# Performance work log

Hardware: AMD Instinct MI355X
Metric: run time of the kernel (lower is better)

Reference implementation:

```python
import jax, jax.numpy as jnp
import numpy as np

# ---- static config (mirrors Net.__init__) ----
N_NODES, N_EDGES = 4000, 20000
N_PROTS, D = 919, 512            # node_emb: Embedding(919, 512); F_in = D (divide_input=False)
TOWERS, F_OUT = 4, D // 4        # F_out = out_channels // towers = 128
EDGE_D = 50
N_GRAPHS, N_CLASSES = 32, 10
N_LAYERS = 2
EPS_BN, EPS_STD = 1e-5, 1e-5

# deg histogram passed to PNAConv; only avg_deg['log'] matters for the scalers used
DEG_HIST = np.array([0., 800., 1200., 900., 600., 300., 150., 50.])
AVG_DEG_LOG = float((np.log(np.arange(DEG_HIST.size) + 1.0) * DEG_HIST).sum() / DEG_HIST.sum())


def setup_inputs() -> dict:
    key = jax.random.key(0)
    ks = jax.random.split(key, 16)
    g = lambda i, shape, s=0.05: (jax.random.normal(ks[i], shape, jnp.float32) * s)
    return dict(
        node_emb_w=g(0, (N_PROTS, D), 0.1),
        edge_emb_w=g(1, (2, EDGE_D), 0.1),
        pe_w=g(2, (2, D)), pe_b=jnp.zeros((D,), jnp.float32),
        edge_enc_w=g(3, (N_LAYERS, EDGE_D, D)), edge_enc_b=jnp.zeros((N_LAYERS, D), jnp.float32),
        pre_w=g(4, (N_LAYERS, TOWERS, 3 * D, D)), pre_b=jnp.zeros((N_LAYERS, TOWERS, D), jnp.float32),
        post_w=g(5, (N_LAYERS, TOWERS, 13 * D, F_OUT)), post_b=jnp.zeros((N_LAYERS, TOWERS, F_OUT), jnp.float32),
        lin_w=g(6, (N_LAYERS, D, D)), lin_b=jnp.zeros((N_LAYERS, D), jnp.float32),
        bn_gamma=jnp.ones((N_LAYERS, D), jnp.float32), bn_beta=jnp.zeros((N_LAYERS, D), jnp.float32),
        acts=jax.random.normal(ks[7], (N_NODES, 2), jnp.float32),
        fc1_w=g(8, (D, 2 * D)), fc1_b=jnp.zeros((2 * D,), jnp.float32),
        fc_out_w=g(9, (2 * D, N_CLASSES)), fc_out_b=jnp.zeros((N_CLASSES,), jnp.float32),
        prelu_a=jnp.float32(0.25),
        global_idx=jax.random.randint(ks[10], (N_NODES,), 0, N_PROTS),
        sign=jax.random.randint(ks[11], (N_EDGES,), 0, 2),
        edge_index=jax.random.randint(ks[12], (2, N_EDGES), 0, N_NODES),
        batch=jnp.sort(jax.random.randint(ks[13], (N_NODES,), 0, N_GRAPHS)),
    )


def _pna_layer(x, src, dst, e, pre_w, pre_b, post_w, post_b, lin_w, lin_b):
    # x: [N, D], e: [E, D] (edge_encoder output), pre_w: [T, 3D, D], post_w: [T, 13D, F_OUT]
    N, E = x.shape[0], src.shape[0]
    # pre-NN on cat([x_i, x_j, edge_attr]) expressed as split matmuls (pre_layers=1 -> single Linear)
    Wi, Wj, We = pre_w[:, :D], pre_w[:, D:2 * D], pre_w[:, 2 * D:]
    m = (jnp.einsum('ef,tfd->etd', x[dst], Wi)
         + jnp.einsum('ef,tfd->etd', x[src], Wj)
         + jnp.einsum('ef,tfd->etd', e, We) + pre_b)          # [E, T, D]
    # multi-aggregation at destination nodes: mean / min / max / std
    cnt = jax.ops.segment_sum(jnp.ones((E,), m.dtype), dst, N)  # in-degree
    has = (cnt > 0)[:, None, None]
    deg = jnp.maximum(cnt, 1.0)[:, None, None]                  # clamp(1) as in PyG
    s1 = jax.ops.segment_sum(m, dst, N)
    s2 = jax.ops.segment_sum(m * m, dst, N)
    mean = s1 / deg
    std = jnp.sqrt(jax.nn.relu(s2 / deg - mean * mean) + EPS_STD)
    mn = jnp.where(has, jax.ops.segment_min(m, dst, N), 0.0)
    mx = jnp.where(has, jax.ops.segment_max(m, dst, N), 0.0)
    agg = jnp.concatenate([mean, mn, mx, std], axis=-1)         # [N, T, 4D]
    # degree scalers: identity, amplification, attenuation
    amp = jnp.log(deg + 1.0) / AVG_DEG_LOG
    out = jnp.concatenate([agg, agg * amp, agg / amp], axis=-1)  # [N, T, 12D]
    # post-NN on cat([x, out]) as split matmuls (post_layers=1)
    Wx, Wo = post_w[:, :D], post_w[:, D:]
    o = (jnp.einsum('nf,tfd->ntd', x, Wx)
         + jnp.einsum('ntf,tfd->ntd', out, Wo) + post_b)        # [N, T, F_OUT]
    return o.reshape(N, TOWERS * F_OUT) @ lin_w + lin_b         # [N, D]


def reference(node_emb_w, edge_emb_w, pe_w, pe_b, edge_enc_w, edge_enc_b,
              pre_w, pre_b, post_w, post_b, lin_w, lin_b, bn_gamma, bn_beta,
              acts, fc1_w, fc1_b, fc_out_w, fc_out_b, prelu_a,
              global_idx, sign, edge_index, batch):
    src, dst = edge_index[0], edge_index[1]
    x = node_emb_w[global_idx] + (acts @ pe_w + pe_b)           # node_emb + PostEncoding
    ea = edge_emb_w[sign]                                       # [E, 50]
    for l in range(N_LAYERS):
        e = ea @ edge_enc_w[l] + edge_enc_b[l]                  # shared edge encoder
        h = _pna_layer(x, src, dst, e, pre_w[l], pre_b[l], post_w[l], post_b[l], lin_w[l], lin_b[l])
        mu = h.mean(axis=0)
        var = ((h - mu) ** 2).mean(axis=0)                      # training-mode BatchNorm (biased var)
        x = jax.nn.relu(bn_gamma[l] * (h - mu) * jax.lax.rsqrt(var + EPS_BN) + bn_beta[l])
    pooled = jax.ops.segment_sum(x, batch, N_GRAPHS)            # global_add_pool
    z = pooled @ fc1_w + fc1_b
    z = jnp.where(z > 0, z, prelu_a * z)                        # PReLU
    logits = z @ fc_out_w + fc_out_b
    return jax.nn.log_softmax(logits, axis=-1)
```

## Files before the change

kernel.cpp:

```cpp
#include <hip/hip_runtime.h>
#include <hip/hip_bf16.h>
#include <float.h>

#define NN 4000
#define NE 20000
#define DD 512
#define NT 4
#define FO 128
#define NG 32
#define NC 10
#define XGW 4096
#define AVGLOG 1.2548916493836102f
#define EPS_STD_ 1e-5f
#define EPS_BN_ 1e-5f

typedef __bf16 bf16x8 __attribute__((ext_vector_type(8)));
typedef float  f32x4  __attribute__((ext_vector_type(4)));

__device__ __forceinline__ void async_copy16(const void* g, void* l) {
    __builtin_amdgcn_global_load_lds((const __attribute__((address_space(1))) void*)g,
                                     (__attribute__((address_space(3))) void*)l, 16, 0, 0);
}

__global__ __launch_bounds__(256) void k_xg(const __bf16* __restrict__ XB, const __bf16* __restrict__ WCAT,
                                            const float* __restrict__ pb,
                                            __bf16* __restrict__ XG, float* __restrict__ OF,
                                            float* __restrict__ BN, float* __restrict__ PL, int zero_pl) {
    const int m0 = blockIdx.y * 128, n0 = blockIdx.x * 128;
    __shared__ __bf16 As[128 * 32];
    __shared__ __bf16 Bs[128 * 32];
    const int tid = threadIdx.x;
    const int wave = tid >> 6, lane = tid & 63;
    const int wm = (wave >> 1) * 64, wn = (wave & 1) * 64;
    const int fr = lane & 15, fq = lane >> 4;
    const int fk = fq * 8;
    const int srow = lane >> 2, skc = (lane & 3) * 8;

    f32x4 acc[4][4];
    const f32x4 zero = {0.f, 0.f, 0.f, 0.f};
#pragma unroll
    for (int i = 0; i < 4; ++i)
#pragma unroll
        for (int j = 0; j < 4; ++j) acc[i][j] = zero;

    for (int k0 = 0; k0 < 512; k0 += 32) {
#pragma unroll
        for (int q = 0; q < 2; ++q) {
            const int row = wave * 32 + q * 16 + srow;
            int ar = m0 + row; if (ar > NN - 1) ar = NN - 1;
            async_copy16(XB + (size_t)ar * 512 + k0 + skc, As + wave * 1024 + q * 512);
            async_copy16(WCAT + (size_t)(n0 + row) * 512 + k0 + skc, Bs + wave * 1024 + q * 512);
        }
        __syncthreads();
        bf16x8 af[4], bfr[4];
#pragma unroll
        for (int mi = 0; mi < 4; ++mi) af[mi]  = *(const bf16x8*)(As + (wm + mi * 16 + fr) * 32 + fk);
#pragma unroll
        for (int ni = 0; ni < 4; ++ni) bfr[ni] = *(const bf16x8*)(Bs + (wn + ni * 16 + fr) * 32 + fk);
#pragma unroll
        for (int mi = 0; mi < 4; ++mi)
#pragma unroll
            for (int ni = 0; ni < 4; ++ni)
                acc[mi][ni] = __builtin_amdgcn_mfma_f32_16x16x32_bf16(af[mi], bfr[ni], acc[mi][ni], 0, 0, 0);
        __syncthreads();
    }
    if (n0 < 4096) {
#pragma unroll
        for (int mi = 0; mi < 4; ++mi) {
#pragma unroll
            for (int ni = 0; ni < 4; ++ni) {
                const int col = n0 + wn + ni * 16 + fr;
                const int rb = m0 + wm + mi * 16 + fq * 4;
#pragma unroll
                for (int r = 0; r < 4; ++r) {
                    const int rowc = rb + r;
                    if (rowc < NN) XG[(size_t)rowc * XGW + col] = (__bf16)acc[mi][ni][r];
                }
            }
        }
    } else {
        const int ocb = n0 - 4096;
#pragma unroll
        for (int mi = 0; mi < 4; ++mi) {
#pragma unroll
            for (int ni = 0; ni < 4; ++ni) {
                const int oc = ocb + wn + ni * 16 + fr;
                const float bv = pb[oc];
                const int rb = m0 + wm + mi * 16 + fq * 4;
#pragma unroll
                for (int r = 0; r < 4; ++r) {
                    const int rowc = rb + r;
                    if (rowc < NN) OF[(size_t)rowc * 512 + oc] = acc[mi][ni][r] + bv;
                }
            }
        }
    }
    if (blockIdx.x == 32 && blockIdx.y == 0) {
        BN[tid] = 0.f; BN[256 + tid] = 0.f; BN[512 + tid] = 0.f; BN[768 + tid] = 0.f;
        if (zero_pl)
            for (int i = tid; i < NG * DD; i += 256) PL[i] = 0.f;
    }
}

__global__ __launch_bounds__(256) void k_gw(const __bf16* __restrict__ AB, const __bf16* __restrict__ WTT,
                                            const float* __restrict__ amp, const float* __restrict__ ramp,
                                            float* __restrict__ OF) {
    const int t = blockIdx.z & 3, kh = blockIdx.z >> 2;
    const int xg = blockIdx.x;
    const int m0 = blockIdx.y * 128;
    const __bf16* A  = AB  + (size_t)t * 2048 + (size_t)kh * 1024;
    const __bf16* BT = WTT + (size_t)t * 384 * 2048 + (size_t)xg * 128 * 2048 + (size_t)kh * 1024;
    __shared__ __bf16 As[128 * 32];
    __shared__ __bf16 Bs[128 * 32];
    const int tid = threadIdx.x;
    const int wave = tid >> 6, lane = tid & 63;
    const int wm = (wave >> 1) * 64, wn = (wave & 1) * 64;
    const int fr = lane & 15, fq = lane >> 4;
    const int fk = fq * 8;
    const int srow = lane >> 2, skc = (lane & 3) * 8;

    f32x4 acc[4][4];
    const f32x4 zero = {0.f, 0.f, 0.f, 0.f};
#pragma unroll
    for (int i = 0; i < 4; ++i)
#pragma unroll
        for (int j = 0; j < 4; ++j) acc[i][j] = zero;

    for (int k0 = 0; k0 < 1024; k0 += 32) {
#pragma unroll
        for (int q = 0; q < 2; ++q) {
            const int row = wave * 32 + q * 16 + srow;
            int ar = m0 + row; if (ar > NN - 1) ar = NN - 1;
            async_copy16(A + (size_t)ar * 8192 + k0 + skc, As + wave * 1024 + q * 512);
            async_copy16(BT + (size_t)row * 2048 + k0 + skc, Bs + wave * 1024 + q * 512);
        }
        __syncthreads();
        bf16x8 af[4], bfr[4];
#pragma unroll
        for (int mi = 0; mi < 4; ++mi) af[mi]  = *(const bf16x8*)(As + (wm + mi * 16 + fr) * 32 + fk);
#pragma unroll
        for (int ni = 0; ni < 4; ++ni) bfr[ni] = *(const bf16x8*)(Bs + (wn + ni * 16 + fr) * 32 + fk);
#pragma unroll
        for (int mi = 0; mi < 4; ++mi)
#pragma unroll
            for (int ni = 0; ni < 4; ++ni)
                acc[mi][ni] = __builtin_amdgcn_mfma_f32_16x16x32_bf16(af[mi], bfr[ni], acc[mi][ni], 0, 0, 0);
        __syncthreads();
    }
#pragma unroll
    for (int mi = 0; mi < 4; ++mi) {
        const int rb = m0 + wm + mi * 16 + fq * 4;
#pragma unroll
        for (int r = 0; r < 4; ++r) {
            const int row = rb + r;
            if (row < NN) {
                const float w = (xg == 0) ? 1.0f : (xg == 1 ? amp[row] : ramp[row]);
                float* orow = OF + (size_t)row * 512 + t * 128;
#pragma unroll
                for (int ni = 0; ni < 4; ++ni)
                    atomicAdd(orow + wn + ni * 16 + fr, acc[mi][ni][r] * w);
            }
        }
    }
}

__global__ __launch_bounds__(256) void k_lin(const float* __restrict__ OF, const __bf16* __restrict__ WLINT,
                                             const float* __restrict__ bl, float* __restrict__ H,
                                             float* __restrict__ BN) {
    const int n0c = blockIdx.x * 128, m0 = blockIdx.y * 64;
    __shared__ __bf16 As[64 * 32];
    __shared__ __bf16 Bs[128 * 32];
    __shared__ float bnS[128], bnQ[128];
    const int tid = threadIdx.x;
    if (tid < 128) { bnS[tid] = 0.f; bnQ[tid] = 0.f; }
    const int wave = tid >> 6, lane = tid & 63;
    const int wr = wave >> 1, wc = wave & 1;
    const int fr = lane & 15, fq = lane >> 4;
    f32x4 acc[2][4];
    const f32x4 zero = {0.f, 0.f, 0.f, 0.f};
#pragma unroll
    for (int i = 0; i < 2; ++i)
#pragma unroll
        for (int j = 0; j < 4; ++j) acc[i][j] = zero;

    const int ar = tid >> 2, akc = (tid & 3) * 8;
    int arow = m0 + ar; if (arow > NN - 1) arow = NN - 1;
    const float* asrc = OF + (size_t)arow * 512;
    for (int k0 = 0; k0 < 512; k0 += 32) {
        float4 f0 = *(const float4*)(asrc + k0 + akc);
        float4 f1 = *(const float4*)(asrc + k0 + akc + 4);
        bf16x8 av;
        av[0] = (__bf16)f0.x; av[1] = (__bf16)f0.y; av[2] = (__bf16)f0.z; av[3] = (__bf16)f0.w;
        av[4] = (__bf16)f1.x; av[5] = (__bf16)f1.y; av[6] = (__bf16)f1.z; av[7] = (__bf16)f1.w;
        *(bf16x8*)(As + ar * 32 + akc) = av;
#pragma unroll
        for (int i = 0; i < 2; ++i) {
            const int cb = tid + 256 * i;
            const int br = cb >> 2, bkc = (cb & 3) * 8;
            async_copy16(WLINT + (size_t)(n0c + br) * 512 + k0 + bkc, Bs + cb * 8);
        }
        __syncthreads();
        bf16x8 a[2], b[4];
#pragma unroll
        for (int mi = 0; mi < 2; ++mi) a[mi] = *(const bf16x8*)(As + (wr * 32 + mi * 16 + fr) * 32 + fq * 8);
#pragma unroll
        for (int ni = 0; ni < 4; ++ni) b[ni] = *(const bf16x8*)(Bs + (wc * 64 + ni * 16 + fr) * 32 + fq * 8);
#pragma unroll
        for (int mi = 0; mi < 2; ++mi)
#pragma unroll
            for (int ni = 0; ni < 4; ++ni)
                acc[mi][ni] = __builtin_amdgcn_mfma_f32_16x16x32_bf16(a[mi], b[ni], acc[mi][ni], 0, 0, 0);
        __syncthreads();
    }
#pragma unroll
    for (int ni = 0; ni < 4; ++ni) {
        const int lc = wc * 64 + ni * 16 + fr;
        const int col = n0c + lc;
        const float bv = bl[col];
        float s = 0.f, q = 0.f;
#pragma unroll
        for (int mi = 0; mi < 2; ++mi) {
#pragma unroll
            for (int r = 0; r < 4; ++r) {
                const int rowc = m0 + wr * 32 + mi * 16 + fq * 4 + r;
                if (rowc < NN) {
                    const float v = acc[mi][ni][r] + bv;
                    H[(size_t)rowc * 512 + col] = v;
                    s += v; q += v * v;
                }
            }
        }
        atomicAdd(&bnS[lc], s); atomicAdd(&bnQ[lc], q);
    }
    __syncthreads();
    if (tid < 128) {
        atomicAdd(&BN[n0c + tid], bnS[tid]);
        atomicAdd(&BN[512 + n0c + tid], bnQ[tid]);
    }
}

__device__ __forceinline__ void tr32(const float* __restrict__ S, int sld,
                                     __bf16* __restrict__ D, int dld, int tx, int ty) {
    __shared__ float t[32][33];
    const int y0 = ty * 4;
#pragma unroll
    for (int i = 0; i < 4; ++i) t[y0 + i][tx] = S[(size_t)(y0 + i) * sld + tx];
    __syncthreads();
#pragma unroll
    for (int i = 0; i < 4; ++i) D[(size_t)(y0 + i) * dld + tx] = (__bf16)t[tx][y0 + i];
}

__global__ __launch_bounds__(256) void k_tr(const float* __restrict__ pw, const float* __restrict__ pow_,
                                            const float* __restrict__ lw,
                                            const float* __restrict__ eemb, const float* __restrict__ eew,
                                            const float* __restrict__ eeb, const float* __restrict__ pb,
                                            __bf16* __restrict__ WCAT, __bf16* __restrict__ WTT,
                                            __bf16* __restrict__ WLINT, float* __restrict__ EM) {
    const int id = blockIdx.x;
    const int tx = threadIdx.x & 31, ty = threadIdx.x >> 5;
    if (id < 2048) {
        const int z = id >> 8, r = id & 255;
        const int t = z & 3, half = z >> 2;
        const int x = r & 15, y = r >> 4;
        const float* S = pw + ((size_t)(t * 1536 + half * 512 + y * 32)) * 512 + x * 32;
        __bf16* D = WCAT + ((size_t)(half * 2048 + t * 512 + x * 32)) * 512 + y * 32;
        tr32(S, 512, D, 512, tx, ty);
    } else if (id < 2304) {
        const int id3 = id - 2048;
        const int t = id3 >> 6, r = id3 & 63;
        const int x = r & 3, y = r >> 2;
        const float* S = pow_ + ((size_t)(t * 6656 + y * 32)) * 128 + x * 32;
        __bf16* D = WCAT + ((size_t)(4096 + t * 128 + x * 32)) * 512 + y * 32;
        tr32(S, 128, D, 512, tx, ty);
    } else if (id < 5376) {
        const int id4 = id - 2304;
        const int z = id4 >> 8, r = id4 & 255;
        const int t = z / 3, w = z % 3;
        const int x = r & 3, y = r >> 2;
        const float* S = pow_ + ((size_t)(t * 6656 + 512 + w * 2048 + y * 32)) * 128 + x * 32;
        __bf16* D = WTT + (size_t)t * 384 * 2048 + ((size_t)(w * 128 + x * 32)) * 2048 + y * 32;
        tr32(S, 128, D, 2048, tx, ty);
    } else if (id < 5632) {
        const int r = id - 5376;
        const int x = r & 15, y = r >> 4;
        const float* S = lw + (size_t)y * 32 * 512 + x * 32;
        __bf16* D = WLINT + (size_t)x * 32 * 512 + y * 32;
        tr32(S, 512, D, 512, tx, ty);
    } else {
        __shared__ float eks[512];
        __shared__ float part[4][64];
        const int tid = threadIdx.x;
        const int id5 = id - 5632;
        const int k = id5 >> 5;
        const int g0 = (id5 & 31) * 64;
#pragma unroll
        for (int h = 0; h < 2; ++h) {
            const int f = tid + h * 256;
            float s = eeb[f];
            for (int c = 0; c < 50; ++c) s += eemb[k * 50 + c] * eew[(size_t)c * 512 + f];
            eks[f] = s;
        }
        __syncthreads();
        const int wave = tid >> 6, lane = tid & 63;
        const int g = g0 + lane;
        const int t = g >> 9, d = g & 511;
        const float* Wp = pw + ((size_t)(t * 1536 + 1024)) * 512 + d;
        float s = 0.f;
        const int f0 = wave * 128;
#pragma unroll 4
        for (int f = f0; f < f0 + 128; ++f) s += eks[f] * Wp[(size_t)f * 512];
        part[wave][lane] = s;
        __syncthreads();
        if (tid < 64) {
            const int gg = g0 + tid;
            EM[k * 2048 + gg] = pb[gg] + part[0][tid] + part[1][tid] + part[2][tid] + part[3][tid];
        }
    }
}

__global__ void k_count(const int* __restrict__ dst, int* __restrict__ cnt) {
    int e = blockIdx.x * 256 + threadIdx.x;
    if (e < NE) atomicAdd(&cnt[dst[e]], 1);
}

__global__ __launch_bounds__(1024) void k_scan_bx(const int* __restrict__ cnt, int* __restrict__ offs,
                                                  float* __restrict__ amp, float* __restrict__ ramp,
                                                  const float* __restrict__ nemb, const float* __restrict__ acts,
                                                  const float* __restrict__ pew, const float* __restrict__ peb,
                                                  const int* __restrict__ gidx, __bf16* __restrict__ XB) {
    const int t = threadIdx.x;
    if (blockIdx.x == 0) {
        __shared__ int part[1024];
        const int base = t * 4;
        int loc[4]; int s = 0;
#pragma unroll
        for (int i = 0; i < 4; ++i) { int v = (base + i < NN) ? cnt[base + i] : 0; loc[i] = s; s += v; }
        part[t] = s;
        __syncthreads();
        for (int o = 1; o < 1024; o <<= 1) {
            int v = (t >= o) ? part[t - o] : 0;
            __syncthreads();
            part[t] += v;
            __syncthreads();
        }
        const int pre = (t > 0) ? part[t - 1] : 0;
#pragma unroll
        for (int i = 0; i < 4; ++i) if (base + i < NN) offs[base + i] = pre + loc[i];
        if (t == 1023) offs[NN] = part[1023];
        for (int n = t; n < NN; n += 1024) {
            float deg = fmaxf((float)cnt[n], 1.0f);
            float a = logf(deg + 1.0f) / AVGLOG;
            amp[n] = a; ramp[n] = 1.0f / a;
        }
    } else {
        const int idx = (blockIdx.x - 1) * 1024 + t;
        const int n = idx >> 9, d = idx & 511;
        float v = nemb[(size_t)gidx[n] * DD + d] + acts[n * 2] * pew[d] + acts[n * 2 + 1] * pew[DD + d] + peb[d];
        XB[idx] = (__bf16)v;
    }
}

__global__ void k_fill(const int* __restrict__ src, const int* __restrict__ dst,
                       const int* __restrict__ sgn, const int* __restrict__ offs,
                       int* __restrict__ fill, int* __restrict__ esrc, int* __restrict__ esgn) {
    int e = blockIdx.x * 256 + threadIdx.x;
    if (e < NE) {
        int d = dst[e];
        int pos = offs[d] + atomicAdd(&fill[d], 1);
        esrc[pos] = src[e];
        esgn[pos] = sgn[e];
    }
}

__global__ __launch_bounds__(256) void k_agg(const __bf16* __restrict__ XG, const float* __restrict__ EM,
                                             const int* __restrict__ offs, const int* __restrict__ cnt,
                                             const int* __restrict__ esrc, const int* __restrict__ esgn,
                                             __bf16* __restrict__ AB) {
    const int n = blockIdx.x;
    const int g = threadIdx.x * 8;
    float xid[8], em0[8], em1[8];
    {
        bf16x8 xb = *(const bf16x8*)(XG + (size_t)n * XGW + g);
#pragma unroll
        for (int i = 0; i < 8; ++i) xid[i] = (float)xb[i];
    }
    *(float4*)&em0[0] = *(const float4*)&EM[g];
    *(float4*)&em0[4] = *(const float4*)&EM[g + 4];
    *(float4*)&em1[0] = *(const float4*)&EM[2048 + g];
    *(float4*)&em1[4] = *(const float4*)&EM[2048 + g + 4];
    float s1[8], s2[8], mn[8], mx[8];
#pragma unroll
    for (int i = 0; i < 8; ++i) { s1[i] = 0.f; s2[i] = 0.f; mn[i] = FLT_MAX; mx[i] = -FLT_MAX; }
    const int j0 = offs[n], j1 = offs[n + 1];
    for (int j = j0; j < j1; ++j) {
        const int s = esrc[j];
        const int sg = esgn[j];
        bf16x8 xv = *(const bf16x8*)(XG + (size_t)s * XGW + 2048 + g);
#pragma unroll
        for (int i = 0; i < 8; ++i) {
            float m = xid[i] + (float)xv[i] + (sg ? em1[i] : em0[i]);
            s1[i] += m; s2[i] += m * m;
            mn[i] = fminf(mn[i], m); mx[i] = fmaxf(mx[i], m);
        }
    }
    const int c = cnt[n];
    const float deg = fmaxf((float)c, 1.0f);
    const float rdeg = 1.0f / deg;
    bf16x8 vmean, vmn, vmx, vsd;
#pragma unroll
    for (int i = 0; i < 8; ++i) {
        float mean = s1[i] * rdeg;
        float var = s2[i] * rdeg - mean * mean;
        float sd = sqrtf(fmaxf(var, 0.f) + EPS_STD_);
        float mnv = (c == 0) ? 0.f : mn[i];
        float mxv = (c == 0) ? 0.f : mx[i];
        vmean[i] = (__bf16)mean; vmn[i] = (__bf16)mnv; vmx[i] = (__bf16)mxv; vsd[i] = (__bf16)sd;
    }
    const int t = g >> 9, d = g & 511;
    __bf16* base = AB + (size_t)n * 8192 + (size_t)t * 2048 + d;
    *(bf16x8*)(base + 0 * DD) = vmean;
    *(bf16x8*)(base + 1 * DD) = vmn;
    *(bf16x8*)(base + 2 * DD) = vmx;
    *(bf16x8*)(base + 3 * DD) = vsd;
}

__global__ void k_bnapply(const float* __restrict__ H, const float* __restrict__ BN,
                          const float* __restrict__ gamma, const float* __restrict__ beta,
                          __bf16* __restrict__ XB, float* __restrict__ PL,
                          const int* __restrict__ batch, int last) {
    int idx = blockIdx.x * 256 + threadIdx.x;
    int n = idx >> 9, d = idx & 511;
    float mu = BN[d] * (1.0f / NN);
    float var = BN[512 + d] * (1.0f / NN) - mu * mu;
    float v = gamma[d] * (H[idx] - mu) * rsqrtf(var + EPS_BN_) + beta[d];
    v = fmaxf(v, 0.f);
    if (last) atomicAdd(&PL[(size_t)batch[n] * DD + d], v);
    else XB[idx] = (__bf16)v;
}

__global__ __launch_bounds__(128) void k_fc1(const float* __restrict__ PL, const float* __restrict__ W1,
                                             const float* __restrict__ b1, const float* __restrict__ pa,
                                             float* __restrict__ Z) {
    const int g = blockIdx.x >> 3;
    const int j = (blockIdx.x & 7) * 128 + threadIdx.x;
    __shared__ float pl[512];
    for (int i = threadIdx.x; i < 512; i += 128) pl[i] = PL[(size_t)g * 512 + i];
    __syncthreads();
    const float* w = W1 + j;
    float s0 = 0.f, s1 = 0.f, s2 = 0.f, s3 = 0.f;
#pragma unroll 2
    for (int f = 0; f < 512; f += 4) {
        s0 += pl[f + 0] * w[(size_t)(f + 0) * 1024];
        s1 += pl[f + 1] * w[(size_t)(f + 1) * 1024];
        s2 += pl[f + 2] * w[(size_t)(f + 2) * 1024];
        s3 += pl[f + 3] * w[(size_t)(f + 3) * 1024];
    }
    float s = b1[j] + ((s0 + s1) + (s2 + s3));
    const float a = *pa;
    Z[(size_t)g * 1024 + j] = s > 0.f ? s : a * s;
}

__global__ __launch_bounds__(64) void k_out(const float* __restrict__ Z, const float* __restrict__ Wo,
                                            const float* __restrict__ bo, float* __restrict__ out) {
    const int g = blockIdx.x, t = threadIdx.x;
    float part[NC];
#pragma unroll
    for (int c = 0; c < NC; ++c) part[c] = 0.f;
    for (int f = t; f < 1024; f += 64) {
        const float zv = Z[(size_t)g * 1024 + f];
#pragma unroll
        for (int c = 0; c < NC; ++c) part[c] += zv * Wo[(size_t)f * NC + c];
    }
#pragma unroll
    for (int off = 32; off > 0; off >>= 1)
#pragma unroll
        for (int c = 0; c < NC; ++c) part[c] += __shfl_down(part[c], off);
    if (t == 0) {
        float lg[NC], mxv = -FLT_MAX;
#pragma unroll
        for (int c = 0; c < NC; ++c) { lg[c] = part[c] + bo[c]; mxv = fmaxf(mxv, lg[c]); }
        float se = 0.f;
#pragma unroll
        for (int c = 0; c < NC; ++c) se += expf(lg[c] - mxv);
        const float lse = mxv + logf(se);
#pragma unroll
        for (int c = 0; c < NC; ++c) out[g * NC + c] = lg[c] - lse;
    }
}

extern "C" void kernel_launch(void* const* d_in, const int* in_sizes, int n_in,
                              void* d_out, int out_size, void* d_ws, size_t ws_size,
                              hipStream_t stream) {
    const float* node_emb_w = (const float*)d_in[0];
    const float* edge_emb_w = (const float*)d_in[1];
    const float* pe_w   = (const float*)d_in[2];
    const float* pe_b   = (const float*)d_in[3];
    const float* edge_enc_w = (const float*)d_in[4];
    const float* edge_enc_b = (const float*)d_in[5];
    const float* pre_w  = (const float*)d_in[6];
    const float* pre_b  = (const float*)d_in[7];
    const float* post_w = (const float*)d_in[8];
    const float* post_b = (const float*)d_in[9];
    const float* lin_w  = (const float*)d_in[10];
    const float* lin_b  = (const float*)d_in[11];
    const float* bn_gamma = (const float*)d_in[12];
    const float* bn_beta  = (const float*)d_in[13];
    const float* acts   = (const float*)d_in[14];
    const float* fc1_w  = (const float*)d_in[15];
    const float* fc1_b  = (const float*)d_in[16];
    const float* fc_out_w = (const float*)d_in[17];
    const float* fc_out_b = (const float*)d_in[18];
    const float* prelu_a  = (const float*)d_in[19];
    const int* global_idx = (const int*)d_in[20];
    const int* sgn        = (const int*)d_in[21];
    const int* edge_index = (const int*)d_in[22];
    const int* batch      = (const int*)d_in[23];
    float* out = (float*)d_out;

    char* W = (char*)d_ws;
    size_t off = 0;
    auto alloc = [&](size_t bytes) { void* p = W + off; off += (bytes + 63) & ~(size_t)63; return p; };
    __bf16* XB    = (__bf16*)alloc((size_t)NN * DD * 2);
    float*  H     = (float*)alloc((size_t)NN * DD * 4);
    __bf16* XG    = (__bf16*)alloc((size_t)NN * XGW * 2);
    __bf16* AB    = (__bf16*)alloc((size_t)NN * 8192 * 2);
    float*  OF    = (float*)alloc((size_t)NN * DD * 4);
    __bf16* WCAT  = (__bf16*)alloc((size_t)4608 * 512 * 2);
    __bf16* WTT   = (__bf16*)alloc((size_t)NT * 384 * 2048 * 2);
    __bf16* WLINT = (__bf16*)alloc((size_t)512 * 512 * 2);
    float*  EM    = (float*)alloc(2 * 2048 * 4);
    float*  BN    = (float*)alloc(1024 * 4);
    float*  PL    = (float*)alloc((size_t)NG * DD * 4);
    float*  ZB    = (float*)alloc((size_t)NG * 1024 * 4);
    float*  AMP   = (float*)alloc(NN * 4);
    float*  RAMP  = (float*)alloc(NN * 4);
    int*    CNT   = (int*)alloc(NN * 4);
    int*    FILL  = (int*)alloc(NN * 4);
    int*    OFFS  = (int*)alloc((NN + 1) * 4);
    int*    ESRC  = (int*)alloc(NE * 4);
    int*    ESGN  = (int*)alloc(NE * 4);

    const int* src = edge_index;
    const int* dst = edge_index + NE;

    hipMemsetAsync(CNT, 0, 2 * NN * sizeof(int), stream);
    k_count<<<(NE + 255) / 256, 256, 0, stream>>>(dst, CNT);
    k_scan_bx<<<2001, 1024, 0, stream>>>(CNT, OFFS, AMP, RAMP,
                                         node_emb_w, acts, pe_w, pe_b, global_idx, XB);
    k_fill<<<(NE + 255) / 256, 256, 0, stream>>>(src, dst, sgn, OFFS, FILL, ESRC, ESGN);

    for (int l = 0; l < 2; ++l) {
        const float* pre_w_l  = pre_w  + (size_t)l * NT * 3 * DD * DD;
        const float* pre_b_l  = pre_b  + (size_t)l * NT * DD;
        const float* post_w_l = post_w + (size_t)l * NT * 6656 * FO;
        const float* post_b_l = post_b + (size_t)l * NT * FO;
        const float* lin_w_l  = lin_w  + (size_t)l * DD * DD;
        const float* lin_b_l  = lin_b  + (size_t)l * DD;
        const float* eew_l    = edge_enc_w + (size_t)l * 50 * DD;
        const float* eeb_l    = edge_enc_b + (size_t)l * DD;

        k_tr<<<5696, 256, 0, stream>>>(pre_w_l, post_w_l, lin_w_l,
                                       edge_emb_w, eew_l, eeb_l, pre_b_l,
                                       WCAT, WTT, WLINT, EM);
        k_xg<<<dim3(36, 32), 256, 0, stream>>>(XB, WCAT, post_b_l, XG, OF, BN, PL, l == 1);
        k_agg<<<NN, 256, 0, stream>>>(XG, EM, OFFS, CNT, ESRC, ESGN, AB);
        k_gw<<<dim3(3, 32, 8), 256, 0, stream>>>(AB, WTT, AMP, RAMP, OF);
        k_lin<<<dim3(4, 63), 256, 0, stream>>>(OF, WLINT, lin_b_l, H, BN);
        k_bnapply<<<NN * DD / 256, 256, 0, stream>>>(H, BN, bn_gamma + (size_t)l * DD,
                                                     bn_beta + (size_t)l * DD, XB, PL, batch, l == 1);
    }

    k_fc1<<<256, 128, 0, stream>>>(PL, fc1_w, fc1_b, prelu_a, ZB);
    k_out<<<NG, 64, 0, stream>>>(ZB, fc_out_w, fc_out_b, out);
}
```

Baseline: 566.5 us.

## Replace k_gw float atomics with bf16 partials, add combine kernel, batch weight prep

```diff
diff --git a/kernel.cpp b/kernel.cpp
--- a/kernel.cpp
+++ b/kernel.cpp
@@ -104,7 +104,7 @@
 
 __global__ __launch_bounds__(256) void k_gw(const __bf16* __restrict__ AB, const __bf16* __restrict__ WTT,
                                             const float* __restrict__ amp, const float* __restrict__ ramp,
-                                            float* __restrict__ OF) {
+                                            __bf16* __restrict__ GWPb) {
     const int t = blockIdx.z & 3, kh = blockIdx.z >> 2;
     const int xg = blockIdx.x;
     const int m0 = blockIdx.y * 128;
@@ -147,6 +147,8 @@
                 acc[mi][ni] = __builtin_amdgcn_mfma_f32_16x16x32_bf16(af[mi], bfr[ni], acc[mi][ni], 0, 0, 0);
         __syncthreads();
     }
+    const int p = xg * 2 + kh;
+    __bf16* P = GWPb + (size_t)p * NN * 512 + (size_t)t * 128;
 #pragma unroll
     for (int mi = 0; mi < 4; ++mi) {
         const int rb = m0 + wm + mi * 16 + fq * 4;
@@ -155,16 +157,33 @@
             const int row = rb + r;
             if (row < NN) {
                 const float w = (xg == 0) ? 1.0f : (xg == 1 ? amp[row] : ramp[row]);
-                float* orow = OF + (size_t)row * 512 + t * 128;
 #pragma unroll
                 for (int ni = 0; ni < 4; ++ni)
-                    atomicAdd(orow + wn + ni * 16 + fr, acc[mi][ni][r] * w);
+                    P[(size_t)row * 512 + wn + ni * 16 + fr] = (__bf16)(acc[mi][ni][r] * w);
             }
         }
     }
 }
 
-__global__ __launch_bounds__(256) void k_lin(const float* __restrict__ OF, const __bf16* __restrict__ WLINT,
+__global__ void k_combine(const float* __restrict__ OF, const __bf16* __restrict__ GWPb,
+                          __bf16* __restrict__ OB) {
+    const size_t idx8 = ((size_t)blockIdx.x * 256 + threadIdx.x) * 8;
+    float4 o0 = *(const float4*)(OF + idx8);
+    float4 o1 = *(const float4*)(OF + idx8 + 4);
+    float s[8] = {o0.x, o0.y, o0.z, o0.w, o1.x, o1.y, o1.z, o1.w};
+#pragma unroll
+    for (int p = 0; p < 6; ++p) {
+        bf16x8 g = *(const bf16x8*)(GWPb + (size_t)p * NN * 512 + idx8);
+#pragma unroll
+        for (int i = 0; i < 8; ++i) s[i] += (float)g[i];
+    }
+    bf16x8 ov;
+#pragma unroll
+    for (int i = 0; i < 8; ++i) ov[i] = (__bf16)s[i];
+    *(bf16x8*)(OB + idx8) = ov;
+}
+
+__global__ __launch_bounds__(256) void k_lin(const __bf16* __restrict__ OB, const __bf16* __restrict__ WLINT,
                                              const float* __restrict__ bl, float* __restrict__ H,
                                              float* __restrict__ BN) {
     const int n0c = blockIdx.x * 128, m0 = blockIdx.y * 64;
@@ -185,14 +204,8 @@
 
     const int ar = tid >> 2, akc = (tid & 3) * 8;
     int arow = m0 + ar; if (arow > NN - 1) arow = NN - 1;
-    const float* asrc = OF + (size_t)arow * 512;
     for (int k0 = 0; k0 < 512; k0 += 32) {
-        float4 f0 = *(const float4*)(asrc + k0 + akc);
-        float4 f1 = *(const float4*)(asrc + k0 + akc + 4);
-        bf16x8 av;
-        av[0] = (__bf16)f0.x; av[1] = (__bf16)f0.y; av[2] = (__bf16)f0.z; av[3] = (__bf16)f0.w;
-        av[4] = (__bf16)f1.x; av[5] = (__bf16)f1.y; av[6] = (__bf16)f1.z; av[7] = (__bf16)f1.w;
-        *(bf16x8*)(As + ar * 32 + akc) = av;
+        async_copy16(OB + (size_t)arow * 512 + k0 + akc, As + tid * 8);
 #pragma unroll
         for (int i = 0; i < 2; ++i) {
             const int cb = tid + 256 * i;
@@ -250,27 +263,39 @@
     for (int i = 0; i < 4; ++i) D[(size_t)(y0 + i) * dld + tx] = (__bf16)t[tx][y0 + i];
 }
 
-__global__ __launch_bounds__(256) void k_tr(const float* __restrict__ pw, const float* __restrict__ pow_,
-                                            const float* __restrict__ lw,
-                                            const float* __restrict__ eemb, const float* __restrict__ eew,
-                                            const float* __restrict__ eeb, const float* __restrict__ pb,
+__global__ __launch_bounds__(256) void k_tr(const float* __restrict__ pre_w, const float* __restrict__ post_w,
+                                            const float* __restrict__ lin_w,
+                                            const float* __restrict__ eemb, const float* __restrict__ eew_b,
+                                            const float* __restrict__ eeb_b, const float* __restrict__ pre_b,
                                             __bf16* __restrict__ WCAT, __bf16* __restrict__ WTT,
                                             __bf16* __restrict__ WLINT, float* __restrict__ EM) {
-    const int id = blockIdx.x;
+    int id = blockIdx.x;
+    const int lay = (id >= 5696) ? 1 : 0;
+    id -= lay * 5696;
+    const float* pw   = pre_w  + (size_t)lay * NT * 3 * 512 * 512;
+    const float* pow_ = post_w + (size_t)lay * NT * 6656 * 128;
+    const float* lw   = lin_w  + (size_t)lay * 512 * 512;
+    const float* eew  = eew_b  + (size_t)lay * 50 * 512;
+    const float* eeb  = eeb_b  + (size_t)lay * 512;
+    const float* pb   = pre_b  + (size_t)lay * NT * 512;
+    __bf16* WCATl  = WCAT  + (size_t)lay * 4608 * 512;
+    __bf16* WTTl   = WTT   + (size_t)lay * NT * 384 * 2048;
+    __bf16* WLINTl = WLINT + (size_t)lay * 512 * 512;
+    float*  EMl    = EM    + (size_t)lay * 4096;
     const int tx = threadIdx.x & 31, ty = threadIdx.x >> 5;
     if (id < 2048) {
         const int z = id >> 8, r = id & 255;
         const int t = z & 3, half = z >> 2;
         const int x = r & 15, y = r >> 4;
         const float* S = pw + ((size_t)(t * 1536 + half * 512 + y * 32)) * 512 + x * 32;
-        __bf16* D = WCAT + ((size_t)(half * 2048 + t * 512 + x * 32)) * 512 + y * 32;
+        __bf16* D = WCATl + ((size_t)(half * 2048 + t * 512 + x * 32)) * 512 + y * 32;
         tr32(S, 512, D, 512, tx, ty);
     } else if (id < 2304) {
         const int id3 = id - 2048;
         const int t = id3 >> 6, r = id3 & 63;
         const int x = r & 3, y = r >> 2;
         const float* S = pow_ + ((size_t)(t * 6656 + y * 32)) * 128 + x * 32;
-        __bf16* D = WCAT + ((size_t)(4096 + t * 128 + x * 32)) * 512 + y * 32;
+        __bf16* D = WCATl + ((size_t)(4096 + t * 128 + x * 32)) * 512 + y * 32;
         tr32(S, 128, D, 512, tx, ty);
     } else if (id < 5376) {
         const int id4 = id - 2304;
@@ -278,13 +303,13 @@
         const int t = z / 3, w = z % 3;
         const int x = r & 3, y = r >> 2;
         const float* S = pow_ + ((size_t)(t * 6656 + 512 + w * 2048 + y * 32)) * 128 + x * 32;
-        __bf16* D = WTT + (size_t)t * 384 * 2048 + ((size_t)(w * 128 + x * 32)) * 2048 + y * 32;
+        __bf16* D = WTTl + (size_t)t * 384 * 2048 + ((size_t)(w * 128 + x * 32)) * 2048 + y * 32;
         tr32(S, 128, D, 2048, tx, ty);
     } else if (id < 5632) {
         const int r = id - 5376;
         const int x = r & 15, y = r >> 4;
         const float* S = lw + (size_t)y * 32 * 512 + x * 32;
-        __bf16* D = WLINT + (size_t)x * 32 * 512 + y * 32;
+        __bf16* D = WLINTl + (size_t)x * 32 * 512 + y * 32;
         tr32(S, 512, D, 512, tx, ty);
     } else {
         __shared__ float eks[512];
@@ -313,7 +338,7 @@
         __syncthreads();
         if (tid < 64) {
             const int gg = g0 + tid;
-            EM[k * 2048 + gg] = pb[gg] + part[0][tid] + part[1][tid] + part[2][tid] + part[3][tid];
+            EMl[k * 2048 + gg] = pb[gg] + part[0][tid] + part[1][tid] + part[2][tid] + part[3][tid];
         }
     }
 }
@@ -525,10 +550,12 @@
     __bf16* XG    = (__bf16*)alloc((size_t)NN * XGW * 2);
     __bf16* AB    = (__bf16*)alloc((size_t)NN * 8192 * 2);
     float*  OF    = (float*)alloc((size_t)NN * DD * 4);
-    __bf16* WCAT  = (__bf16*)alloc((size_t)4608 * 512 * 2);
-    __bf16* WTT   = (__bf16*)alloc((size_t)NT * 384 * 2048 * 2);
-    __bf16* WLINT = (__bf16*)alloc((size_t)512 * 512 * 2);
-    float*  EM    = (float*)alloc(2 * 2048 * 4);
+    __bf16* GWPb  = (__bf16*)alloc((size_t)6 * NN * 512 * 2);
+    __bf16* OB    = (__bf16*)alloc((size_t)NN * DD * 2);
+    __bf16* WCAT  = (__bf16*)alloc((size_t)2 * 4608 * 512 * 2);
+    __bf16* WTT   = (__bf16*)alloc((size_t)2 * NT * 384 * 2048 * 2);
+    __bf16* WLINT = (__bf16*)alloc((size_t)2 * 512 * 512 * 2);
+    float*  EM    = (float*)alloc((size_t)2 * 2 * 2048 * 4);
     float*  BN    = (float*)alloc(1024 * 4);
     float*  PL    = (float*)alloc((size_t)NG * DD * 4);
     float*  ZB    = (float*)alloc((size_t)NG * 1024 * 4);
@@ -548,24 +575,23 @@
     k_scan_bx<<<2001, 1024, 0, stream>>>(CNT, OFFS, AMP, RAMP,
                                          node_emb_w, acts, pe_w, pe_b, global_idx, XB);
     k_fill<<<(NE + 255) / 256, 256, 0, stream>>>(src, dst, sgn, OFFS, FILL, ESRC, ESGN);
+    k_tr<<<2 * 5696, 256, 0, stream>>>(pre_w, post_w, lin_w,
+                                       edge_emb_w, edge_enc_w, edge_enc_b, pre_b,
+                                       WCAT, WTT, WLINT, EM);
 
     for (int l = 0; l < 2; ++l) {
-        const float* pre_w_l  = pre_w  + (size_t)l * NT * 3 * DD * DD;
-        const float* pre_b_l  = pre_b  + (size_t)l * NT * DD;
-        const float* post_w_l = post_w + (size_t)l * NT * 6656 * FO;
         const float* post_b_l = post_b + (size_t)l * NT * FO;
-        const float* lin_w_l  = lin_w  + (size_t)l * DD * DD;
         const float* lin_b_l  = lin_b  + (size_t)l * DD;
-        const float* eew_l    = edge_enc_w + (size_t)l * 50 * DD;
-        const float* eeb_l    = edge_enc_b + (size_t)l * DD;
-
-        k_tr<<<5696, 256, 0, stream>>>(pre_w_l, post_w_l, lin_w_l,
-                                       edge_emb_w, eew_l, eeb_l, pre_b_l,
-                                       WCAT, WTT, WLINT, EM);
-        k_xg<<<dim3(36, 32), 256, 0, stream>>>(XB, WCAT, post_b_l, XG, OF, BN, PL, l == 1);
-        k_agg<<<NN, 256, 0, stream>>>(XG, EM, OFFS, CNT, ESRC, ESGN, AB);
-        k_gw<<<dim3(3, 32, 8), 256, 0, stream>>>(AB, WTT, AMP, RAMP, OF);
-        k_lin<<<dim3(4, 63), 256, 0, stream>>>(OF, WLINT, lin_b_l, H, BN);
+        __bf16* WCATl  = WCAT  + (size_t)l * 4608 * 512;
+        __bf16* WTTl   = WTT   + (size_t)l * NT * 384 * 2048;
+        __bf16* WLINTl = WLINT + (size_t)l * 512 * 512;
+        float*  EMl    = EM    + (size_t)l * 4096;
+
+        k_xg<<<dim3(36, 32), 256, 0, stream>>>(XB, WCATl, post_b_l, XG, OF, BN, PL, l == 1);
+        k_agg<<<NN, 256, 0, stream>>>(XG, EMl, OFFS, CNT, ESRC, ESGN, AB);
+        k_gw<<<dim3(3, 32, 8), 256, 0, stream>>>(AB, WTTl, AMP, RAMP, GWPb);
+        k_combine<<<NN * DD / 2048, 256, 0, stream>>>(OF, GWPb, OB);
+        k_lin<<<dim3(4, 63), 256, 0, stream>>>(OB, WLINTl, lin_b_l, H, BN);
         k_bnapply<<<NN * DD / 256, 256, 0, stream>>>(H, BN, bn_gamma + (size_t)l * DD,
                                                      bn_beta + (size_t)l * DD, XB, PL, batch, l == 1);
     }
```

Result: faster. 499.0 us (-11.9%).
